# Kernel optimization log

Measured on AMD Instinct MI355X. Metric: run time of the kernel, lower is better.

Reference implementation:

```python
import jax, jax.numpy as jnp
import numpy as np

B, C, W, H = 4, 256, 64, 64
DK = 32


def setup_inputs() -> dict:
    key = jax.random.key(0)
    ks = jax.random.split(key, 5)
    x = jax.random.normal(ks[0], (B, C, W, H), dtype=jnp.float32)
    # 1x1 conv weights ~ linear projections; scale like conv default init
    s = 1.0 / np.sqrt(C)
    Wq = jax.random.normal(ks[1], (DK, C), dtype=jnp.float32) * s
    Wk = jax.random.normal(ks[2], (DK, C), dtype=jnp.float32) * s
    Wv = jax.random.normal(ks[3], (C, C), dtype=jnp.float32) * s
    bq = jnp.zeros((DK,), jnp.float32)
    bk = jnp.zeros((DK,), jnp.float32)
    bv = jnp.zeros((C,), jnp.float32)
    # NOTE: module initializes gamma=0 (output == x, zero grads to Q/K/V);
    # use a nonzero value so the attention path is exercised.
    gamma = jax.random.uniform(ks[4], (1,), dtype=jnp.float32) + 0.5
    return {"x": x, "Wq": Wq, "bq": bq, "Wk": Wk, "bk": bk,
            "Wv": Wv, "bv": bv, "gamma": gamma}


def reference(x, Wq, bq, Wk, bk, Wv, bv, gamma):
    b, c, w, h = x.shape
    n = w * h
    xf = x.reshape(b, c, n)                      # [B, C, N]
    q = jnp.einsum('kc,bcn->bkn', Wq, xf) + bq[None, :, None]  # [B, dk, N]
    k = jnp.einsum('kc,bcn->bkn', Wk, xf) + bk[None, :, None]  # [B, dk, N]
    v = jnp.einsum('oc,bcn->bon', Wv, xf) + bv[None, :, None]  # [B, C, N]
    energy = jnp.einsum('bkn,bkm->bnm', q, k)    # [B, N, N] (no 1/sqrt(dk) scale)
    attn = jax.nn.softmax(energy, axis=-1)       # softmax over keys m
    # out[b,c,n] = sum_m v[b,c,m] * attn[b,n,m]  (bmm(V, A^T))
    out = jnp.einsum('bcm,bnm->bcn', v, attn)
    out = out.reshape(b, c, w, h)
    out = gamma[0] * out + x                      # channel_in == channel_out
    return out
```

## Files before the change

kernel.cpp:

```cpp
#include <hip/hip_runtime.h>
#include <hip/hip_bf16.h>
#include <stdint.h>

typedef float f32x16 __attribute__((ext_vector_type(16)));
typedef short bf16x8 __attribute__((ext_vector_type(8)));

#define L2E 1.4426950408889634f
#define ROWPAT(r, hi) (((r) & 3) + 8 * ((r) >> 2) + 4 * (hi))

#define WCATB_OFF 0u
#define XT_OFF    163840u
#define QBUF_OFF  8552448u
#define KBUF_OFF  9601024u
#define VBUF_OFF  10649600u

static __device__ __forceinline__ ushort f2bf(float f) {
    union { float f; uint32_t u; } v; v.f = f;
    uint32_t u = v.u;
    return (ushort)((u + 0x7fffu + ((u >> 16) & 1u)) >> 16);
}

static __device__ __forceinline__ uint32_t cvtpk(float lo, float hi) {
    uint32_t r;
    asm volatile("v_cvt_pk_bf16_f32 %0, %1, %2" : "=v"(r) : "v"(lo), "v"(hi));
    return r;
}
static __device__ __forceinline__ bf16x8 packP(float p0, float p1, float p2, float p3,
                                               float p4, float p5, float p6, float p7) {
    uint32_t a0 = cvtpk(p0, p1), a1 = cvtpk(p2, p3);
    uint32_t b0 = cvtpk(p4, p5), b1 = cvtpk(p6, p7);
    auto s0 = __builtin_amdgcn_permlane32_swap(a0, b0, false, false);
    auto s1 = __builtin_amdgcn_permlane32_swap(a1, b1, false, false);
    union { uint32_t u[4]; bf16x8 v; } pk;
    pk.u[0] = s0[0];
    pk.u[1] = s1[0];
    pk.u[2] = s0[1];
    pk.u[3] = s1[1];
    return pk.v;
}

__global__ void prep_kernel(const float* __restrict__ Wq, const float* __restrict__ Wk,
                            const float* __restrict__ Wv, ushort* __restrict__ Wcb) {
    int row = blockIdx.x, c = threadIdx.x;
    float v;
    if (row < 32)      v = Wq[row * 256 + c];
    else if (row < 64) v = Wk[(row - 32) * 256 + c];
    else               v = Wv[(row - 64) * 256 + c];
    Wcb[row * 256 + c] = f2bf(v);
}

__global__ __launch_bounds__(256)
void xt_kernel(const float* __restrict__ x, ushort* __restrict__ xT) {
    __shared__ ushort t[64][80];
    const int tid = threadIdx.x;
    const int b = blockIdx.x >> 8;
    const int c0 = ((blockIdx.x >> 6) & 3) << 6;
    const int n0 = (blockIdx.x & 63) << 6;
    const float* xb = x + ((size_t)(b * 256 + c0)) * 4096 + n0;
    #pragma unroll
    for (int p = 0; p < 4; ++p) {
        int cl = (tid >> 4) + p * 16;
        int nl = (tid & 15) * 4;
        float4 v = *(const float4*)(xb + (size_t)cl * 4096 + nl);
        t[nl + 0][cl] = f2bf(v.x);
        t[nl + 1][cl] = f2bf(v.y);
        t[nl + 2][cl] = f2bf(v.z);
        t[nl + 3][cl] = f2bf(v.w);
    }
    __syncthreads();
    ushort* xo = xT + ((size_t)(b * 4096 + n0)) * 256 + c0;
    #pragma unroll
    for (int p = 0; p < 2; ++p) {
        int idx = tid + (p << 8);
        int nl = idx >> 3, sg = idx & 7;
        *(uint4*)(xo + (size_t)nl * 256 + sg * 8) = *(const uint4*)&t[nl][sg * 8];
    }
}

__global__ __launch_bounds__(256)
void proj_qk_kernel(const ushort* __restrict__ xT, const ushort* __restrict__ Wcb,
                    const float* __restrict__ bq, const float* __restrict__ bk,
                    ushort* __restrict__ qbuf, ushort* __restrict__ kbuf) {
    const int tid = threadIdx.x;
    const int w = tid >> 6, l31 = tid & 31, hi = (tid & 63) >> 5;
    const int b = blockIdx.x >> 5;
    const int nt = (blockIdx.x & 31) * 4 + w;

    const ushort* xrow = xT + ((size_t)(b * 4096 + nt * 32 + l31)) * 256;
    const ushort* wq = Wcb + (size_t)l31 * 256;
    const ushort* wk = Wcb + (size_t)(32 + l31) * 256;

    f32x16 accQ = (f32x16)0.0f, accK = (f32x16)0.0f;
    #pragma unroll
    for (int kk = 0; kk < 16; ++kk) {
        bf16x8 af = *(const bf16x8*)&xrow[kk * 16 + hi * 8];
        bf16x8 bq8 = *(const bf16x8*)&wq[kk * 16 + hi * 8];
        bf16x8 bk8 = *(const bf16x8*)&wk[kk * 16 + hi * 8];
        accQ = __builtin_amdgcn_mfma_f32_32x32x16_bf16(af, bq8, accQ, 0, 0, 0);
        accK = __builtin_amdgcn_mfma_f32_32x32x16_bf16(af, bk8, accK, 0, 0, 0);
    }
    const float bqv = bq[l31], bkv = bk[l31];
    #pragma unroll
    for (int r = 0; r < 16; ++r) {
        int n = nt * 32 + ROWPAT(r, hi);
        qbuf[((size_t)((b << 12) + n)) * 32 + l31] = f2bf(accQ[r] + bqv);
        kbuf[((size_t)((b << 12) + n)) * 32 + l31] = f2bf(accK[r] + bkv);
    }
}

__global__ __launch_bounds__(256)
void proj_v_kernel(const ushort* __restrict__ xT, const ushort* __restrict__ Wcb,
                   const float* __restrict__ bv, ushort* __restrict__ vbuf) {
    const int tid = threadIdx.x;
    const int w = tid >> 6, l31 = tid & 31, hi = (tid & 63) >> 5;
    const int b = blockIdx.x >> 8;
    const int ct = (blockIdx.x >> 5) & 7;
    const int nt = (blockIdx.x & 31) * 4 + w;

    const ushort* wv = Wcb + (size_t)(64 + ct * 32 + l31) * 256;
    const ushort* xrow = xT + ((size_t)(b * 4096 + nt * 32 + l31)) * 256;

    f32x16 acc = (f32x16)0.0f;
    #pragma unroll
    for (int kk = 0; kk < 16; ++kk) {
        bf16x8 af = *(const bf16x8*)&wv[kk * 16 + hi * 8];
        bf16x8 bf8 = *(const bf16x8*)&xrow[kk * 16 + hi * 8];
        acc = __builtin_amdgcn_mfma_f32_32x32x16_bf16(af, bf8, acc, 0, 0, 0);
    }
    #pragma unroll
    for (int r = 0; r < 16; ++r) {
        int c = ct * 32 + ROWPAT(r, hi);
        vbuf[((size_t)(b * 256 + c)) * 4096 + nt * 32 + l31] = f2bf(acc[r] + bv[c]);
    }
}

#define KSTR 40
#define VSTR 72
__global__ __launch_bounds__(512)
void attn_kernel(const ushort* __restrict__ qbuf, const ushort* __restrict__ kbuf,
                 const ushort* __restrict__ vbuf, const float* __restrict__ x,
                 const float* __restrict__ gammap, float* __restrict__ out) {
    __shared__ ushort klds[2][64 * KSTR];
    __shared__ ushort vlds[2][256 * VSTR];
    __shared__ float  dlds[2][2][32];

    const int tid = threadIdx.x;
    const int bid = blockIdx.x;
    const int work = (bid & 7) * 32 + (bid >> 3);
    const int b = work >> 6;
    const int qbase = (work & 63) << 6;
    const int w = tid >> 6, l = tid & 63;
    const int l31 = l & 31, hi = l >> 5;
    const int qt = w >> 2, kh = (w >> 1) & 1, cp = w & 1;

    const ushort* kb = kbuf + ((size_t)b << 12) * 32;
    const ushort* vb = vbuf + ((size_t)b << 8) * 4096;

    const ushort* qrow = qbuf + ((size_t)((b << 12) + qbase + qt * 32 + l31)) * 32;
    const bf16x8 qf0 = *(const bf16x8*)&qrow[hi * 8];
    const bf16x8 qf1 = *(const bf16x8*)&qrow[16 + hi * 8];

    f32x16 acc[4];
    #pragma unroll
    for (int ch = 0; ch < 4; ++ch) acc[ch] = (f32x16)0.0f;
    float dsum = 0.f;

    const int vc = tid >> 3, vs = tid & 7;
    const int krow = tid >> 2, kseg = tid & 3;
    uint4 vreg[4], kreg;

    #pragma unroll
    for (int i = 0; i < 4; ++i)
        vreg[i] = *(const uint4*)(vb + (size_t)(vc + 64 * i) * 4096 + vs * 8);
    if (tid < 256) kreg = *(const uint4*)(kb + (size_t)krow * 32 + kseg * 8);
    #pragma unroll
    for (int i = 0; i < 4; ++i)
        *(uint4*)&vlds[0][(vc + 64 * i) * VSTR + vs * 8] = vreg[i];
    if (tid < 256) *(uint4*)&klds[0][krow * KSTR + kseg * 8] = kreg;
    __syncthreads();

    for (int it = 0; it < 64; ++it) {
        const int cur = it & 1;
        if (it < 63) {
            const int m0 = (it + 1) << 6;
            #pragma unroll
            for (int i = 0; i < 4; ++i)
                vreg[i] = *(const uint4*)(vb + (size_t)(vc + 64 * i) * 4096 + m0 + vs * 8);
            if (tid < 256) kreg = *(const uint4*)(kb + (size_t)(m0 + krow) * 32 + kseg * 8);
        }

        const int krow_a = (kh * 32 + l31) * KSTR;
        bf16x8 kf0 = *(const bf16x8*)&klds[cur][krow_a + hi * 8];
        bf16x8 kf1 = *(const bf16x8*)&klds[cur][krow_a + 16 + hi * 8];
        f32x16 sT = __builtin_amdgcn_mfma_f32_32x32x16_bf16(kf0, qf0, (f32x16)0.0f, 0, 0, 0);
        sT = __builtin_amdgcn_mfma_f32_32x32x16_bf16(kf1, qf1, sT, 0, 0, 0);

        float p[16];
        #pragma unroll
        for (int r = 0; r < 16; ++r) {
            p[r] = exp2f(sT[r] * L2E);
            dsum += p[r];
        }
        bf16x8 pf0 = packP(p[0], p[1], p[2], p[3], p[4], p[5], p[6], p[7]);
        bf16x8 pf1 = packP(p[8], p[9], p[10], p[11], p[12], p[13], p[14], p[15]);

        #pragma unroll
        for (int ch = 0; ch < 4; ++ch) {
            const int crow = (cp * 128 + ch * 32 + l31) * VSTR + kh * 32;
            bf16x8 vfa = *(const bf16x8*)&vlds[cur][crow + hi * 8];
            bf16x8 vfb = *(const bf16x8*)&vlds[cur][crow + 16 + hi * 8];
            acc[ch] = __builtin_amdgcn_mfma_f32_32x32x16_bf16(vfa, pf0, acc[ch], 0, 0, 0);
            acc[ch] = __builtin_amdgcn_mfma_f32_32x32x16_bf16(vfb, pf1, acc[ch], 0, 0, 0);
        }

        if (it < 63) {
            const int nb = cur ^ 1;
            #pragma unroll
            for (int i = 0; i < 4; ++i)
                *(uint4*)&vlds[nb][(vc + 64 * i) * VSTR + vs * 8] = vreg[i];
            if (tid < 256) *(uint4*)&klds[nb][krow * KSTR + kseg * 8] = kreg;
        }
        __syncthreads();
    }

    const float gam = gammap[0];
    float dall = dsum + __shfl_xor(dsum, 32);
    float* scr = (float*)&vlds[0][0];
    if (kh == 1) {
        #pragma unroll
        for (int ch = 0; ch < 4; ++ch)
            #pragma unroll
            for (int r = 0; r < 16; ++r)
                scr[((((qt * 2 + cp) * 4 + ch) * 16 + r) << 6) + l] = acc[ch][r];
    }
    if (cp == 0 && l < 32) dlds[qt][kh][l31] = dall;
    __syncthreads();
    if (kh == 0) {
        const float denom = dlds[qt][0][l31] + dlds[qt][1][l31];
        const float ginv = gam / denom;
        const float* xb = x + (((size_t)b) << 8) * 4096;
        float* ob = out + (((size_t)b) << 8) * 4096;
        const int q = qbase + qt * 32 + l31;
        #pragma unroll
        for (int ch = 0; ch < 4; ++ch) {
            #pragma unroll
            for (int r = 0; r < 16; ++r) {
                int c = cp * 128 + ch * 32 + ROWPAT(r, hi);
                float o = acc[ch][r] + scr[((((qt * 2 + cp) * 4 + ch) * 16 + r) << 6) + l];
                size_t idx = (size_t)c * 4096 + q;
                ob[idx] = o * ginv + xb[idx];
            }
        }
    }
}

extern "C" void kernel_launch(void* const* d_in, const int* in_sizes, int n_in,
                              void* d_out, int out_size, void* d_ws, size_t ws_size,
                              hipStream_t stream) {
    (void)in_sizes; (void)n_in; (void)out_size; (void)ws_size;
    const float* x     = (const float*)d_in[0];
    const float* Wq    = (const float*)d_in[1];
    const float* bq    = (const float*)d_in[2];
    const float* Wk    = (const float*)d_in[3];
    const float* bk    = (const float*)d_in[4];
    const float* Wv    = (const float*)d_in[5];
    const float* bv    = (const float*)d_in[6];
    const float* gamma = (const float*)d_in[7];
    float* out = (float*)d_out;

    char* ws = (char*)d_ws;
    ushort* Wcb  = (ushort*)(ws + WCATB_OFF);
    ushort* xT   = (ushort*)(ws + XT_OFF);
    ushort* qbuf = (ushort*)(ws + QBUF_OFF);
    ushort* kbuf = (ushort*)(ws + KBUF_OFF);
    ushort* vbuf = (ushort*)(ws + VBUF_OFF);

    prep_kernel<<<320, 256, 0, stream>>>(Wq, Wk, Wv, Wcb);
    xt_kernel<<<1024, 256, 0, stream>>>(x, xT);
    proj_qk_kernel<<<128, 256, 0, stream>>>(xT, Wcb, bq, bk, qbuf, kbuf);
    proj_v_kernel<<<1024, 256, 0, stream>>>(xT, Wcb, bv, vbuf);
    attn_kernel<<<256, 512, 0, stream>>>(qbuf, kbuf, vbuf, x, gamma, out);
}
```

Baseline: 129.6 us.

## Specialize attention waves into QK/softmax producers and PV consumers via LDS

```diff
diff --git a/kernel.cpp b/kernel.cpp
--- a/kernel.cpp
+++ b/kernel.cpp
@@ -25,18 +25,18 @@
     asm volatile("v_cvt_pk_bf16_f32 %0, %1, %2" : "=v"(r) : "v"(lo), "v"(hi));
     return r;
 }
-static __device__ __forceinline__ bf16x8 packP(float p0, float p1, float p2, float p3,
-                                               float p4, float p5, float p6, float p7) {
+static __device__ __forceinline__ uint4 packP(float p0, float p1, float p2, float p3,
+                                              float p4, float p5, float p6, float p7) {
     uint32_t a0 = cvtpk(p0, p1), a1 = cvtpk(p2, p3);
     uint32_t b0 = cvtpk(p4, p5), b1 = cvtpk(p6, p7);
     auto s0 = __builtin_amdgcn_permlane32_swap(a0, b0, false, false);
     auto s1 = __builtin_amdgcn_permlane32_swap(a1, b1, false, false);
-    union { uint32_t u[4]; bf16x8 v; } pk;
-    pk.u[0] = s0[0];
-    pk.u[1] = s1[0];
-    pk.u[2] = s0[1];
-    pk.u[3] = s1[1];
-    return pk.v;
+    uint4 pk;
+    pk.x = s0[0];
+    pk.y = s1[0];
+    pk.z = s0[1];
+    pk.w = s1[1];
+    return pk;
 }
 
 __global__ void prep_kernel(const float* __restrict__ Wq, const float* __restrict__ Wk,
@@ -83,28 +83,26 @@
                     ushort* __restrict__ qbuf, ushort* __restrict__ kbuf) {
     const int tid = threadIdx.x;
     const int w = tid >> 6, l31 = tid & 31, hi = (tid & 63) >> 5;
-    const int b = blockIdx.x >> 5;
-    const int nt = (blockIdx.x & 31) * 4 + w;
+    const int b = blockIdx.x >> 6;
+    const int nt = (blockIdx.x & 63) * 2 + (w & 1);
+    const int isK = w >> 1;
 
     const ushort* xrow = xT + ((size_t)(b * 4096 + nt * 32 + l31)) * 256;
-    const ushort* wq = Wcb + (size_t)l31 * 256;
-    const ushort* wk = Wcb + (size_t)(32 + l31) * 256;
-
-    f32x16 accQ = (f32x16)0.0f, accK = (f32x16)0.0f;
+    const ushort* wrow = Wcb + (size_t)(isK * 32 + l31) * 256;
+
+    f32x16 acc = (f32x16)0.0f;
     #pragma unroll
     for (int kk = 0; kk < 16; ++kk) {
         bf16x8 af = *(const bf16x8*)&xrow[kk * 16 + hi * 8];
-        bf16x8 bq8 = *(const bf16x8*)&wq[kk * 16 + hi * 8];
-        bf16x8 bk8 = *(const bf16x8*)&wk[kk * 16 + hi * 8];
-        accQ = __builtin_amdgcn_mfma_f32_32x32x16_bf16(af, bq8, accQ, 0, 0, 0);
-        accK = __builtin_amdgcn_mfma_f32_32x32x16_bf16(af, bk8, accK, 0, 0, 0);
-    }
-    const float bqv = bq[l31], bkv = bk[l31];
+        bf16x8 bf8 = *(const bf16x8*)&wrow[kk * 16 + hi * 8];
+        acc = __builtin_amdgcn_mfma_f32_32x32x16_bf16(af, bf8, acc, 0, 0, 0);
+    }
+    const float bias = isK ? bk[l31] : bq[l31];
+    ushort* dst = isK ? kbuf : qbuf;
     #pragma unroll
     for (int r = 0; r < 16; ++r) {
         int n = nt * 32 + ROWPAT(r, hi);
-        qbuf[((size_t)((b << 12) + n)) * 32 + l31] = f2bf(accQ[r] + bqv);
-        kbuf[((size_t)((b << 12) + n)) * 32 + l31] = f2bf(accK[r] + bkv);
+        dst[((size_t)((b << 12) + n)) * 32 + l31] = f2bf(acc[r] + bias);
     }
 }
 
@@ -141,7 +139,8 @@
                  const ushort* __restrict__ vbuf, const float* __restrict__ x,
                  const float* __restrict__ gammap, float* __restrict__ out) {
     __shared__ ushort klds[2][64 * KSTR];
-    __shared__ ushort vlds[2][256 * VSTR];
+    __shared__ ushort vlds[3][256 * VSTR];
+    __shared__ uint4  plds[2 * 2 * 2 * 2 * 64];
     __shared__ float  dlds[2][2][32];
 
     const int tid = threadIdx.x;
@@ -151,7 +150,9 @@
     const int qbase = (work & 63) << 6;
     const int w = tid >> 6, l = tid & 63;
     const int l31 = l & 31, hi = l >> 5;
-    const int qt = w >> 2, kh = (w >> 1) & 1, cp = w & 1;
+    const bool isQK = (w < 4);
+    const int qt = isQK ? (w >> 1) : ((w - 4) >> 1);
+    const int khcp = w & 1;
 
     const ushort* kb = kbuf + ((size_t)b << 12) * 32;
     const ushort* vb = vbuf + ((size_t)b << 8) * 4096;
@@ -167,88 +168,106 @@
 
     const int vc = tid >> 3, vs = tid & 7;
     const int krow = tid >> 2, kseg = tid & 3;
+    const ushort* vsrc = vb + (size_t)vc * 4096 + vs * 8;
+    const ushort* ksrc = kb + (size_t)krow * 32 + kseg * 8;
     uint4 vreg[4], kreg;
 
     #pragma unroll
     for (int i = 0; i < 4; ++i)
-        vreg[i] = *(const uint4*)(vb + (size_t)(vc + 64 * i) * 4096 + vs * 8);
-    if (tid < 256) kreg = *(const uint4*)(kb + (size_t)krow * 32 + kseg * 8);
+        vreg[i] = *(const uint4*)(vsrc + (size_t)i * 64 * 4096);
+    if (tid < 256) kreg = *(const uint4*)ksrc;
     #pragma unroll
     for (int i = 0; i < 4; ++i)
         *(uint4*)&vlds[0][(vc + 64 * i) * VSTR + vs * 8] = vreg[i];
     if (tid < 256) *(uint4*)&klds[0][krow * KSTR + kseg * 8] = kreg;
     __syncthreads();
 
-    for (int it = 0; it < 64; ++it) {
+    int vw = 1, vr = 2;
+    for (int it = 0; it <= 64; ++it) {
         const int cur = it & 1;
+
         if (it < 63) {
-            const int m0 = (it + 1) << 6;
+            const size_t m0 = (size_t)(it + 1) << 6;
             #pragma unroll
             for (int i = 0; i < 4; ++i)
-                vreg[i] = *(const uint4*)(vb + (size_t)(vc + 64 * i) * 4096 + m0 + vs * 8);
-            if (tid < 256) kreg = *(const uint4*)(kb + (size_t)(m0 + krow) * 32 + kseg * 8);
+                vreg[i] = *(const uint4*)(vsrc + (size_t)i * 64 * 4096 + m0);
+            if (tid < 256) kreg = *(const uint4*)(ksrc + (m0 << 5));
         }
 
-        const int krow_a = (kh * 32 + l31) * KSTR;
-        bf16x8 kf0 = *(const bf16x8*)&klds[cur][krow_a + hi * 8];
-        bf16x8 kf1 = *(const bf16x8*)&klds[cur][krow_a + 16 + hi * 8];
-        f32x16 sT = __builtin_amdgcn_mfma_f32_32x32x16_bf16(kf0, qf0, (f32x16)0.0f, 0, 0, 0);
-        sT = __builtin_amdgcn_mfma_f32_32x32x16_bf16(kf1, qf1, sT, 0, 0, 0);
-
-        float p[16];
-        #pragma unroll
-        for (int r = 0; r < 16; ++r) {
-            p[r] = exp2f(sT[r] * L2E);
-            dsum += p[r];
+        if (isQK) {
+            if (it < 64) {
+                const int krow_a = (khcp * 32 + l31) * KSTR;
+                bf16x8 kf0 = *(const bf16x8*)&klds[cur][krow_a + hi * 8];
+                bf16x8 kf1 = *(const bf16x8*)&klds[cur][krow_a + 16 + hi * 8];
+                f32x16 sT = __builtin_amdgcn_mfma_f32_32x32x16_bf16(kf0, qf0, (f32x16)0.0f, 0, 0, 0);
+                sT = __builtin_amdgcn_mfma_f32_32x32x16_bf16(kf1, qf1, sT, 0, 0, 0);
+
+                float p[16];
+                #pragma unroll
+                for (int r = 0; r < 16; ++r) {
+                    p[r] = exp2f(sT[r] * L2E);
+                    dsum += p[r];
+                }
+                uint4 w0 = packP(p[0], p[1], p[2], p[3], p[4], p[5], p[6], p[7]);
+                uint4 w1 = packP(p[8], p[9], p[10], p[11], p[12], p[13], p[14], p[15]);
+                uint4* pb = &plds[(((cur * 2 + qt) * 2 + khcp) * 2) * 64];
+                pb[l] = w0;
+                pb[64 + l] = w1;
+            } else {
+                float dall = dsum + __shfl_xor(dsum, 32);
+                if (l < 32) dlds[qt][khcp][l31] = dall;
+            }
+        } else {
+            if (it >= 1) {
+                const uint4* pb = &plds[(((cur ^ 1) * 2 + qt) * 2) * 2 * 64];
+                union { uint4 u; bf16x8 v; } pf[4];
+                pf[0].u = pb[l];
+                pf[1].u = pb[64 + l];
+                pf[2].u = pb[128 + l];
+                pf[3].u = pb[192 + l];
+                const ushort* vt = &vlds[vr][0];
+                #pragma unroll
+                for (int ch = 0; ch < 4; ++ch) {
+                    const int crow = (khcp * 128 + ch * 32 + l31) * VSTR;
+                    bf16x8 vfa = *(const bf16x8*)&vt[crow + hi * 8];
+                    bf16x8 vfb = *(const bf16x8*)&vt[crow + 16 + hi * 8];
+                    bf16x8 vfc = *(const bf16x8*)&vt[crow + 32 + hi * 8];
+                    bf16x8 vfd = *(const bf16x8*)&vt[crow + 48 + hi * 8];
+                    acc[ch] = __builtin_amdgcn_mfma_f32_32x32x16_bf16(vfa, pf[0].v, acc[ch], 0, 0, 0);
+                    acc[ch] = __builtin_amdgcn_mfma_f32_32x32x16_bf16(vfb, pf[1].v, acc[ch], 0, 0, 0);
+                    acc[ch] = __builtin_amdgcn_mfma_f32_32x32x16_bf16(vfc, pf[2].v, acc[ch], 0, 0, 0);
+                    acc[ch] = __builtin_amdgcn_mfma_f32_32x32x16_bf16(vfd, pf[3].v, acc[ch], 0, 0, 0);
+                }
+            }
         }
-        bf16x8 pf0 = packP(p[0], p[1], p[2], p[3], p[4], p[5], p[6], p[7]);
-        bf16x8 pf1 = packP(p[8], p[9], p[10], p[11], p[12], p[13], p[14], p[15]);
-
-        #pragma unroll
-        for (int ch = 0; ch < 4; ++ch) {
-            const int crow = (cp * 128 + ch * 32 + l31) * VSTR + kh * 32;
-            bf16x8 vfa = *(const bf16x8*)&vlds[cur][crow + hi * 8];
-            bf16x8 vfb = *(const bf16x8*)&vlds[cur][crow + 16 + hi * 8];
-            acc[ch] = __builtin_amdgcn_mfma_f32_32x32x16_bf16(vfa, pf0, acc[ch], 0, 0, 0);
-            acc[ch] = __builtin_amdgcn_mfma_f32_32x32x16_bf16(vfb, pf1, acc[ch], 0, 0, 0);
-        }
 
         if (it < 63) {
-            const int nb = cur ^ 1;
             #pragma unroll
             for (int i = 0; i < 4; ++i)
-                *(uint4*)&vlds[nb][(vc + 64 * i) * VSTR + vs * 8] = vreg[i];
-            if (tid < 256) *(uint4*)&klds[nb][krow * KSTR + kseg * 8] = kreg;
+                *(uint4*)&vlds[vw][(vc + 64 * i) * VSTR + vs * 8] = vreg[i];
+            if (tid < 256) *(uint4*)&klds[cur ^ 1][krow * KSTR + kseg * 8] = kreg;
         }
-        __syncthreads();
-    }
-
-    const float gam = gammap[0];
-    float dall = dsum + __shfl_xor(dsum, 32);
-    float* scr = (float*)&vlds[0][0];
-    if (kh == 1) {
-        #pragma unroll
-        for (int ch = 0; ch < 4; ++ch)
-            #pragma unroll
-            for (int r = 0; r < 16; ++r)
-                scr[((((qt * 2 + cp) * 4 + ch) * 16 + r) << 6) + l] = acc[ch][r];
-    }
-    if (cp == 0 && l < 32) dlds[qt][kh][l31] = dall;
+        if (it < 64) __syncthreads();
+        vw = (vw == 2) ? 0 : vw + 1;
+        vr = (vr == 2) ? 0 : vr + 1;
+    }
+
     __syncthreads();
-    if (kh == 0) {
+
+    if (!isQK) {
+        const float gam = gammap[0];
         const float denom = dlds[qt][0][l31] + dlds[qt][1][l31];
         const float ginv = gam / denom;
-        const float* xb = x + (((size_t)b) << 8) * 4096;
+        const float* xb2 = x + (((size_t)b) << 8) * 4096;
         float* ob = out + (((size_t)b) << 8) * 4096;
         const int q = qbase + qt * 32 + l31;
         #pragma unroll
         for (int ch = 0; ch < 4; ++ch) {
             #pragma unroll
             for (int r = 0; r < 16; ++r) {
-                int c = cp * 128 + ch * 32 + ROWPAT(r, hi);
-                float o = acc[ch][r] + scr[((((qt * 2 + cp) * 4 + ch) * 16 + r) << 6) + l];
+                int c = khcp * 128 + ch * 32 + ROWPAT(r, hi);
                 size_t idx = (size_t)c * 4096 + q;
-                ob[idx] = o * ginv + xb[idx];
+                ob[idx] = acc[ch][r] * ginv + xb2[idx];
             }
         }
     }
@@ -277,7 +296,7 @@
 
     prep_kernel<<<320, 256, 0, stream>>>(Wq, Wk, Wv, Wcb);
     xt_kernel<<<1024, 256, 0, stream>>>(x, xT);
-    proj_qk_kernel<<<128, 256, 0, stream>>>(xT, Wcb, bq, bk, qbuf, kbuf);
+    proj_qk_kernel<<<256, 256, 0, stream>>>(xT, Wcb, bq, bk, qbuf, kbuf);
     proj_v_kernel<<<1024, 256, 0, stream>>>(xT, Wcb, bv, vbuf);
     attn_kernel<<<256, 512, 0, stream>>>(qbuf, kbuf, vbuf, x, gamma, out);
 }
```

New measurement: 197.0 us. 1.52x slower.
